# Kernel optimization log

Measured on AMD Instinct MI355X. Metric: run time of the kernel, lower is better.

Reference implementation:

```python
import jax, jax.numpy as jnp
import numpy as np

N, IN_RAW, H, E, UNROLLS = 1024, 10, 96, 16384, 2

def _p(key, shape):
    return jax.random.normal(key, shape, dtype=jnp.float32) * 0.05

def setup_inputs() -> dict:
    key = jax.random.key(0)
    ks = jax.random.split(key, 24)
    x = jax.random.normal(ks[0], (N, IN_RAW), dtype=jnp.float32)
    edge_index = jax.random.randint(ks[1], (2, E), 0, N, dtype=jnp.int64)
    adj = jax.random.randint(ks[2], (N, N), 0, 2, dtype=jnp.int32)
    return {
        'x': x, 'edge_index': edge_index, 'adj': adj,
        # init_layer
        'W_init': _p(ks[3], (H, IN_RAW - 1)), 'b_init': _p(ks[4], (H,)),
        # GatedGraphConv (num_layers=1): weight [H,H], GRUCell params
        'W_ggc': _p(ks[5], (H, H)),
        'W_ih': _p(ks[6], (3 * H, H)), 'W_hh': _p(ks[7], (3 * H, H)),
        'b_ih': _p(ks[8], (3 * H,)), 'b_hh': _p(ks[9], (3 * H,)),
        # edge_attention: Linear(2H->H), Linear(H->1)
        'Wa1': _p(ks[10], (H, 2 * H)), 'ba1': _p(ks[11], (H,)),
        'Wa2': _p(ks[12], (1, H)), 'ba2': _p(ks[13], (1,)),
        # out MLP
        'Wo1': _p(ks[14], (H, H)), 'bo1': _p(ks[15], (H,)),
        'Wo2': _p(ks[16], (H, H)), 'bo2': _p(ks[17], (H,)),
        # heads
        'Wp1': _p(ks[18], (1, H)), 'bp1': _p(ks[19], (1,)),
        'Wp2': _p(ks[20], (1, H)), 'bp2': _p(ks[21], (1,)),
    }

def _leaky(v):
    return jnp.where(v >= 0, v, 0.01 * v)  # LeakyReLU default slope

def _ggnn_forward(x, edge_index, adj,
                  W_init, b_init, W_ggc, W_ih, W_hh, b_ih, b_hh,
                  Wa1, ba1, Wa2, ba2, Wo1, bo1, Wo2, bo2,
                  Wp1, bp1, Wp2, bp2):
    src, tgt = edge_index[0], edge_index[1]
    x = x[:, :-1]                                   # data.x[:, :-1]
    x = _leaky(x @ W_init.T + b_init)               # [N,H]
    adj_mask = (adj == 1)
    for _ in range(UNROLLS):
        # GatedGraphConv, 1 layer, aggr='mean'
        m = x @ W_ggc                               # [N,H]
        s = jax.ops.segment_sum(m[src], tgt, num_segments=N)
        cnt = jax.ops.segment_sum(jnp.ones((E,), x.dtype), tgt, num_segments=N)
        agg = s / jnp.maximum(cnt, 1.0)[:, None]    # mean, 0 for isolated nodes
        # GRUCell(agg, x)
        gi = agg @ W_ih.T + b_ih
        gh = x @ W_hh.T + b_hh
        ir, iz, inn = jnp.split(gi, 3, axis=1)
        hr, hz, hn = jnp.split(gh, 3, axis=1)
        r = jax.nn.sigmoid(ir + hr)
        z = jax.nn.sigmoid(iz + hz)
        n = jnp.tanh(inn + r * hn)
        x = (1.0 - z) * n + z * x
        # edge attention: concat(x_i, x_j) -> Linear(2H->H) decomposed into
        # two [H,H] halves so the NxNx2H concat tensor is never materialized.
        hi = x @ Wa1[:, :H].T                       # acts on t1 (row i)
        hj = x @ Wa1[:, H:].T                       # acts on t2 (row j)
        h = jax.nn.sigmoid(hi[:, None, :] + hj[None, :, :] + ba1)  # [N,N,H]
        coeffs = jax.nn.sigmoid(h @ Wa2[0] + ba2[0])               # [N,N]
        coeffs = jnp.where(adj_mask, coeffs, 0.0)
        x = coeffs @ x
    x = _leaky(x @ Wo1.T + bo1)
    x = _leaky(x @ Wo2.T + bo2)
    out1 = jax.nn.sigmoid(x @ Wp1.T + bp1)
    out2 = jax.nn.sigmoid(x @ Wp2.T + bp2)
    return out1, out2

def reference(x, edge_index, adj,
              W_init, b_init, W_ggc, W_ih, W_hh, b_ih, b_hh,
              Wa1, ba1, Wa2, ba2, Wo1, bo1, Wo2, bo2,
              Wp1, bp1, Wp2, bp2):
    return _ggnn_forward(x, edge_index, adj,
                         W_init, b_init, W_ggc, W_ih, W_hh, b_ih, b_hh,
                         Wa1, ba1, Wa2, ba2, Wo1, bo1, Wo2, bo2,
                         Wp1, bp1, Wp2, bp2)
```

## Files before the change

kernel.cpp:

```cpp
#include <hip/hip_runtime.h>

#define Nn 1024
#define Hh 96
#define Ee 16384
#define IN_K 9
#define IN_STRIDE 10
#define NH (Nn * Hh)
#define XS 128
#define SLOTS 64

__device__ __forceinline__ float sigf(float v) {
    return __builtin_amdgcn_rcpf(1.0f + __expf(-v));
}
__device__ __forceinline__ float tanhfast(float v) {
    float e = __expf(2.0f * v);
    return (e - 1.0f) * __builtin_amdgcn_rcpf(e + 1.0f);
}
__device__ __forceinline__ float leakyf(float v) {
    return v >= 0.0f ? v : 0.01f * v;
}

__global__ __launch_bounds__(256) void setup1_kernel(
    const float* __restrict__ W_ih, const float* __restrict__ W_hh,
    const float* __restrict__ Wa1, const float* __restrict__ Wo1,
    const float* __restrict__ Wo2, const float* __restrict__ x_in,
    const float* __restrict__ W_init, const float* __restrict__ b_init,
    float* __restrict__ Wt_ih, float* __restrict__ Wt_hh,
    float* __restrict__ Wt_a1i, float* __restrict__ Wt_a1j,
    float* __restrict__ Wt_o1, float* __restrict__ Wt_o2,
    int* __restrict__ deg, float* __restrict__ xA)
{
    int gt = blockIdx.x * 256 + threadIdx.x;
    if (gt < Nn) deg[gt] = 0;
    if (gt < 92160) {
        int idx = gt;
        if (idx < 27648) {
            int k = idx / 288, c = idx % 288;
            Wt_ih[idx] = W_ih[c * 96 + k];
        } else if ((idx -= 27648) < 27648) {
            int k = idx / 288, c = idx % 288;
            Wt_hh[idx] = W_hh[c * 96 + k];
        } else if ((idx -= 27648) < 9216) {
            int k = idx / 96, h = idx % 96;
            Wt_a1i[idx] = Wa1[h * 192 + k];
        } else if ((idx -= 9216) < 9216) {
            int k = idx / 96, h = idx % 96;
            Wt_a1j[idx] = Wa1[h * 192 + 96 + k];
        } else if ((idx -= 9216) < 9216) {
            int k = idx / 96, j = idx % 96;
            Wt_o1[idx] = Wo1[j * 96 + k];
        } else {
            idx -= 9216;
            int k = idx / 96, j = idx % 96;
            Wt_o2[idx] = Wo2[j * 96 + k];
        }
    }
    if (gt < NH) {
        int n = gt / Hh, j = gt - n * Hh;
        const float* xr = x_in + n * IN_STRIDE;
        const float* wr = W_init + j * IN_K;
        float acc = b_init[j];
#pragma unroll
        for (int k = 0; k < IN_K; ++k) acc += xr[k] * wr[k];
        xA[n * XS + j] = leakyf(acc);
    }
}

__global__ __launch_bounds__(256) void setup2_kernel(
    const int* __restrict__ ei, const float* __restrict__ W_ggc,
    const float* __restrict__ Wt_ih,
    int* __restrict__ deg, int* __restrict__ bucket, float* __restrict__ Wf)
{
    int gt = blockIdx.x * 256 + threadIdx.x;
    if (gt < Ee) {
        int src = ei[gt];
        int tgt = ei[Ee + gt];
        int slot = atomicAdd(&deg[tgt], 1);
        if (slot < SLOTS) bucket[tgt * SLOTS + slot] = src;
    } else if (gt < Ee + 27648) {
        int idx = gt - Ee;
        int k = idx / 288, c = idx % 288;
        const float* g = W_ggc + k * 96;
        const float* w = Wt_ih + c;
        float acc = 0.0f;
        for (int j = 0; j < 96; ++j) acc += g[j] * w[j * 288];
        Wf[idx] = acc;
    }
}

__global__ __launch_bounds__(384) void gru_kernel(
    const float* __restrict__ xA, const int* __restrict__ deg,
    const int* __restrict__ bucket,
    const float* __restrict__ Wf, const float* __restrict__ Wt_hh,
    const float* __restrict__ b_ih, const float* __restrict__ b_hh,
    const float* __restrict__ Wt_a1i, const float* __restrict__ Wt_a1j,
    const float* __restrict__ ba1,
    float* __restrict__ xB, float* __restrict__ Ei, float* __restrict__ EjT)
{
    __shared__ float Pm[4][Hh];
    __shared__ float Xr[4][Hh];
    __shared__ float Xo[4][Hh];
    int tid = threadIdx.x;
    int r = tid / Hh, h = tid - r * Hh;
    int n = blockIdx.x * 4 + r;
    {
        int d = deg[n];
        int dc = d < SLOTS ? d : SLOTS;
        const int* bk = bucket + n * SLOTS;
        float acc = 0.0f;
        for (int s = 0; s < dc; ++s)
            acc += xA[bk[s] * XS + h];
        Pm[r][h] = acc * __builtin_amdgcn_rcpf(fmaxf((float)d, 1.0f));
        Xr[r][h] = xA[n * XS + h];
    }
    __syncthreads();
    {
        const float* Pr = Pm[r];
        const float* xr = Xr[r];
        const float* pf = Wf + h;
        const float* ph = Wt_hh + h;
        float gir = b_ih[h], giz = b_ih[Hh + h], gin = b_ih[2 * Hh + h];
        float ghr = b_hh[h], ghz = b_hh[Hh + h], ghn = b_hh[2 * Hh + h];
        for (int k = 0; k < Hh; ++k) {
            float a = Pr[k];
            float xv = xr[k];
            int o = k * 288;
            gir += a * pf[o];
            giz += a * pf[o + 96];
            gin += a * pf[o + 192];
            ghr += xv * ph[o];
            ghz += xv * ph[o + 96];
            ghn += xv * ph[o + 192];
        }
        float rr = sigf(gir + ghr);
        float z = sigf(giz + ghz);
        float nn2 = tanhfast(gin + rr * ghn);
        float xo = (1.0f - z) * nn2 + z * xr[h];
        xB[n * XS + h] = xo;
        Xo[r][h] = xo;
    }
    __syncthreads();
    {
        const float* row = Xo[r];
        const float* wi = Wt_a1i + h;
        const float* wj = Wt_a1j + h;
        float a = 0.0f, bb = 0.0f;
        for (int k = 0; k < Hh; ++k) {
            float xv = row[k];
            a += xv * wi[k * 96];
            bb += xv * wj[k * 96];
        }
        Ei[n * Hh + h] = __expf(-(a + ba1[h]));
        EjT[h * Nn + n] = __expf(-bb);
    }
}

#define SM_WA2 0
#define SM_EIS 96
#define SM_C   480
#define SM_RED 4576
__global__ __launch_bounds__(512) void attn_kernel(
    const float* __restrict__ Ei, const float* __restrict__ EjT,
    const float* __restrict__ Wa2, const float* __restrict__ ba2,
    const int* __restrict__ adj, const float* __restrict__ xB,
    float* __restrict__ xA)
{
    __shared__ float sm[4576 + 1536];
    int tid = threadIdx.x;
    int i0 = blockIdx.x * 4;
    if (tid < Hh) sm[SM_WA2 + tid] = Wa2[tid];
    if (tid < 4 * Hh) {
        int r = tid / Hh, h = tid - r * Hh;
        sm[SM_EIS + tid] = Ei[(i0 + r) * Hh + h];
    }
    __syncthreads();
    {
        int j2 = tid * 2;
        float a0 = 0.f, a1 = 0.f, a2 = 0.f, a3 = 0.f;
        float b0 = 0.f, b1 = 0.f, b2_ = 0.f, b3 = 0.f;
        const float* eis = sm + SM_EIS;
#pragma unroll 2
        for (int k = 0; k < Hh; ++k) {
            float2 e = *(const float2*)(EjT + k * Nn + j2);
            float wk = sm[SM_WA2 + k];
            float e0 = eis[k];
            float e1 = eis[96 + k];
            float e2 = eis[192 + k];
            float e3 = eis[288 + k];
            a0 += __builtin_amdgcn_rcpf(fmaf(e0, e.x, 1.0f)) * wk;
            b0 += __builtin_amdgcn_rcpf(fmaf(e0, e.y, 1.0f)) * wk;
            a1 += __builtin_amdgcn_rcpf(fmaf(e1, e.x, 1.0f)) * wk;
            b1 += __builtin_amdgcn_rcpf(fmaf(e1, e.y, 1.0f)) * wk;
            a2 += __builtin_amdgcn_rcpf(fmaf(e2, e.x, 1.0f)) * wk;
            b2_ += __builtin_amdgcn_rcpf(fmaf(e2, e.y, 1.0f)) * wk;
            a3 += __builtin_amdgcn_rcpf(fmaf(e3, e.x, 1.0f)) * wk;
            b3 += __builtin_amdgcn_rcpf(fmaf(e3, e.y, 1.0f)) * wk;
        }
        float bb = ba2[0];
        int2 m0 = *(const int2*)(adj + (i0 + 0) * Nn + j2);
        int2 m1 = *(const int2*)(adj + (i0 + 1) * Nn + j2);
        int2 m2 = *(const int2*)(adj + (i0 + 2) * Nn + j2);
        int2 m3 = *(const int2*)(adj + (i0 + 3) * Nn + j2);
        sm[SM_C + 0 * Nn + j2]     = (m0.x == 1) ? sigf(a0 + bb) : 0.0f;
        sm[SM_C + 0 * Nn + j2 + 1] = (m0.y == 1) ? sigf(b0 + bb) : 0.0f;
        sm[SM_C + 1 * Nn + j2]     = (m1.x == 1) ? sigf(a1 + bb) : 0.0f;
        sm[SM_C + 1 * Nn + j2 + 1] = (m1.y == 1) ? sigf(b1 + bb) : 0.0f;
        sm[SM_C + 2 * Nn + j2]     = (m2.x == 1) ? sigf(a2 + bb) : 0.0f;
        sm[SM_C + 2 * Nn + j2 + 1] = (m2.y == 1) ? sigf(b2_ + bb) : 0.0f;
        sm[SM_C + 3 * Nn + j2]     = (m3.x == 1) ? sigf(a3 + bb) : 0.0f;
        sm[SM_C + 3 * Nn + j2 + 1] = (m3.y == 1) ? sigf(b3 + bb) : 0.0f;
    }
    __syncthreads();
    {
        int q = tid >> 7;
        int h = tid & 127;
        float acc0 = 0.f, acc1 = 0.f, acc2 = 0.f, acc3 = 0.f;
        if (h < Hh) {
            const float* xc = xB + h;
            int jb = q * 256;
            const float* c0 = sm + SM_C + 0 * Nn + jb;
            const float* c1 = sm + SM_C + 1 * Nn + jb;
            const float* c2 = sm + SM_C + 2 * Nn + jb;
            const float* c3 = sm + SM_C + 3 * Nn + jb;
#pragma unroll 4
            for (int j = 0; j < 256; ++j) {
                float xv = xc[(jb + j) * XS];
                acc0 += c0[j] * xv;
                acc1 += c1[j] * xv;
                acc2 += c2[j] * xv;
                acc3 += c3[j] * xv;
            }
            sm[SM_RED + (q * 4 + 0) * Hh + h] = acc0;
            sm[SM_RED + (q * 4 + 1) * Hh + h] = acc1;
            sm[SM_RED + (q * 4 + 2) * Hh + h] = acc2;
            sm[SM_RED + (q * 4 + 3) * Hh + h] = acc3;
        }
        __syncthreads();
        if (q == 0 && h < Hh) {
#pragma unroll
            for (int r = 0; r < 4; ++r) {
                float v = sm[SM_RED + r * Hh + h]
                        + sm[SM_RED + (4 + r) * Hh + h]
                        + sm[SM_RED + (8 + r) * Hh + h]
                        + sm[SM_RED + (12 + r) * Hh + h];
                xA[(i0 + r) * XS + h] = v;
            }
        }
    }
}

__global__ __launch_bounds__(384) void head_kernel(
    const float* __restrict__ xA,
    const float* __restrict__ Wt_o1, const float* __restrict__ bo1,
    const float* __restrict__ Wt_o2, const float* __restrict__ bo2,
    const float* __restrict__ Wp1, const float* __restrict__ bp1,
    const float* __restrict__ Wp2, const float* __restrict__ bp2,
    float* __restrict__ out)
{
    __shared__ float xr[4][Hh];
    __shared__ float t1[4][Hh];
    __shared__ float t2[4][Hh];
    int tid = threadIdx.x;
    int r = tid / Hh, h = tid - r * Hh;
    int n = blockIdx.x * 4 + r;
    xr[r][h] = xA[n * XS + h];
    __syncthreads();
    {
        const float* w = Wt_o1 + h;
        float acc = bo1[h];
        for (int k = 0; k < Hh; ++k) acc += xr[r][k] * w[k * 96];
        t1[r][h] = leakyf(acc);
    }
    __syncthreads();
    {
        const float* w = Wt_o2 + h;
        float acc = bo2[h];
        for (int k = 0; k < Hh; ++k) acc += t1[r][k] * w[k * 96];
        t2[r][h] = leakyf(acc);
    }
    __syncthreads();
    if (h == 0) {
        float s1 = 0.f;
        for (int k = 0; k < Hh; ++k) s1 += t2[r][k] * Wp1[k];
        out[n] = sigf(s1 + bp1[0]);
    } else if (h == 1) {
        float s2 = 0.f;
        for (int k = 0; k < Hh; ++k) s2 += t2[r][k] * Wp2[k];
        out[Nn + n] = sigf(s2 + bp2[0]);
    }
}

extern "C" void kernel_launch(void* const* d_in, const int* in_sizes, int n_in,
                              void* d_out, int out_size, void* d_ws, size_t ws_size,
                              hipStream_t stream)
{
    const float* x_in   = (const float*)d_in[0];
    const int*   ei     = (const int*)d_in[1];
    const int*   adj    = (const int*)d_in[2];
    const float* W_init = (const float*)d_in[3];
    const float* b_init = (const float*)d_in[4];
    const float* W_ggc  = (const float*)d_in[5];
    const float* W_ih   = (const float*)d_in[6];
    const float* W_hh   = (const float*)d_in[7];
    const float* b_ih   = (const float*)d_in[8];
    const float* b_hh   = (const float*)d_in[9];
    const float* Wa1    = (const float*)d_in[10];
    const float* ba1    = (const float*)d_in[11];
    const float* Wa2    = (const float*)d_in[12];
    const float* ba2    = (const float*)d_in[13];
    const float* Wo1    = (const float*)d_in[14];
    const float* bo1    = (const float*)d_in[15];
    const float* Wo2    = (const float*)d_in[16];
    const float* bo2    = (const float*)d_in[17];
    const float* Wp1    = (const float*)d_in[18];
    const float* bp1    = (const float*)d_in[19];
    const float* Wp2    = (const float*)d_in[20];
    const float* bp2    = (const float*)d_in[21];
    float* out = (float*)d_out;

    float* ws     = (float*)d_ws;
    float* xA     = ws;
    float* xB     = xA + Nn * XS;
    float* Ei     = xB + Nn * XS;
    float* EjT    = Ei + NH;
    float* Wt_ih  = EjT + NH;
    float* Wt_hh  = Wt_ih + 27648;
    float* Wf     = Wt_hh + 27648;
    float* Wt_a1i = Wf + 27648;
    float* Wt_a1j = Wt_a1i + 9216;
    float* Wt_o1  = Wt_a1j + 9216;
    float* Wt_o2  = Wt_o1 + 9216;
    int*   deg    = (int*)(Wt_o2 + 9216);
    int*   bucket = deg + Nn;

    setup1_kernel<<<(NH + 255) / 256, 256, 0, stream>>>(
        W_ih, W_hh, Wa1, Wo1, Wo2, x_in, W_init, b_init,
        Wt_ih, Wt_hh, Wt_a1i, Wt_a1j, Wt_o1, Wt_o2, deg, xA);
    setup2_kernel<<<(Ee + 27648 + 255) / 256, 256, 0, stream>>>(
        ei, W_ggc, Wt_ih, deg, bucket, Wf);

    for (int u = 0; u < 2; ++u) {
        gru_kernel<<<Nn / 4, 384, 0, stream>>>(
            xA, deg, bucket, Wf, Wt_hh, b_ih, b_hh,
            Wt_a1i, Wt_a1j, ba1, xB, Ei, EjT);
        attn_kernel<<<Nn / 4, 512, 0, stream>>>(
            Ei, EjT, Wa2, ba2, adj, xB, xA);
    }

    head_kernel<<<Nn / 4, 384, 0, stream>>>(
        xA, Wt_o1, bo1, Wt_o2, bo2, Wp1, bp1, Wp2, bp2, out);
}
```

Baseline: 227.8 us.

## Halve rows per block, split GRU reductions, fuse head into attention kernel

Each GRU and attention block now handles 2 nodes instead of 4, so 512 blocks launch instead of 256. The GRU kernel splits its K-reductions and neighbour gathers across two thread halves, combined through shared memory. The head MLP is fused into the final attention launch through a template flag, and Wf is computed directly from W_ih, so the transposed Wt_ih pass and one dependency are dropped. This is meant to raise occupancy and parallelism and cut launch count. In exchange it adds extra syncs and shared-memory reductions, and each EjT load is now reused across 2 rows instead of 4.

```diff
diff --git a/kernel.cpp b/kernel.cpp
--- a/kernel.cpp
+++ b/kernel.cpp
@@ -20,24 +20,22 @@
     return v >= 0.0f ? v : 0.01f * v;
 }
 
-__global__ __launch_bounds__(256) void setup1_kernel(
-    const float* __restrict__ W_ih, const float* __restrict__ W_hh,
-    const float* __restrict__ Wa1, const float* __restrict__ Wo1,
-    const float* __restrict__ Wo2, const float* __restrict__ x_in,
-    const float* __restrict__ W_init, const float* __restrict__ b_init,
-    float* __restrict__ Wt_ih, float* __restrict__ Wt_hh,
-    float* __restrict__ Wt_a1i, float* __restrict__ Wt_a1j,
-    float* __restrict__ Wt_o1, float* __restrict__ Wt_o2,
+__global__ __launch_bounds__(256) void setup_kernel(
+    const float* __restrict__ W_hh, const float* __restrict__ Wa1,
+    const float* __restrict__ Wo1, const float* __restrict__ Wo2,
+    const float* __restrict__ W_ggc, const float* __restrict__ W_ih,
+    const float* __restrict__ x_in, const float* __restrict__ W_init,
+    const float* __restrict__ b_init,
+    float* __restrict__ Wt_hh, float* __restrict__ Wt_a1i,
+    float* __restrict__ Wt_a1j, float* __restrict__ Wt_o1,
+    float* __restrict__ Wt_o2, float* __restrict__ Wf,
     int* __restrict__ deg, float* __restrict__ xA)
 {
     int gt = blockIdx.x * 256 + threadIdx.x;
     if (gt < Nn) deg[gt] = 0;
-    if (gt < 92160) {
+    if (gt < 64512) {
         int idx = gt;
         if (idx < 27648) {
-            int k = idx / 288, c = idx % 288;
-            Wt_ih[idx] = W_ih[c * 96 + k];
-        } else if ((idx -= 27648) < 27648) {
             int k = idx / 288, c = idx % 288;
             Wt_hh[idx] = W_hh[c * 96 + k];
         } else if ((idx -= 27648) < 9216) {
@@ -55,6 +53,14 @@
             Wt_o2[idx] = Wo2[j * 96 + k];
         }
     }
+    if (gt < 27648) {
+        int k = gt / 288, c = gt % 288;
+        const float* g = W_ggc + k * 96;
+        const float* w = W_ih + c * 96;
+        float acc = 0.0f;
+        for (int j = 0; j < 96; ++j) acc += g[j] * w[j];
+        Wf[gt] = acc;
+    }
     if (gt < NH) {
         int n = gt / Hh, j = gt - n * Hh;
         const float* xr = x_in + n * IN_STRIDE;
@@ -66,26 +72,15 @@
     }
 }
 
-__global__ __launch_bounds__(256) void setup2_kernel(
-    const int* __restrict__ ei, const float* __restrict__ W_ggc,
-    const float* __restrict__ Wt_ih,
-    int* __restrict__ deg, int* __restrict__ bucket, float* __restrict__ Wf)
-{
-    int gt = blockIdx.x * 256 + threadIdx.x;
-    if (gt < Ee) {
-        int src = ei[gt];
-        int tgt = ei[Ee + gt];
-        int slot = atomicAdd(&deg[tgt], 1);
-        if (slot < SLOTS) bucket[tgt * SLOTS + slot] = src;
-    } else if (gt < Ee + 27648) {
-        int idx = gt - Ee;
-        int k = idx / 288, c = idx % 288;
-        const float* g = W_ggc + k * 96;
-        const float* w = Wt_ih + c;
-        float acc = 0.0f;
-        for (int j = 0; j < 96; ++j) acc += g[j] * w[j * 288];
-        Wf[idx] = acc;
-    }
+__global__ __launch_bounds__(256) void edges_kernel(
+    const int* __restrict__ ei, int* __restrict__ deg, int* __restrict__ bucket)
+{
+    int e = blockIdx.x * 256 + threadIdx.x;
+    if (e >= Ee) return;
+    int src = ei[e];
+    int tgt = ei[Ee + e];
+    int slot = atomicAdd(&deg[tgt], 1);
+    if (slot < SLOTS) bucket[tgt * SLOTS + slot] = src;
 }
 
 __global__ __launch_bounds__(384) void gru_kernel(
@@ -97,21 +92,31 @@
     const float* __restrict__ ba1,
     float* __restrict__ xB, float* __restrict__ Ei, float* __restrict__ EjT)
 {
-    __shared__ float Pm[4][Hh];
-    __shared__ float Xr[4][Hh];
-    __shared__ float Xo[4][Hh];
+    __shared__ float Pp[2][2][Hh];
+    __shared__ float Pm[2][Hh];
+    __shared__ float Xr[2][Hh];
+    __shared__ float Xo[2][Hh];
+    __shared__ float red6[2][2][Hh][6];
+    __shared__ float redp[2][2][Hh][2];
     int tid = threadIdx.x;
-    int r = tid / Hh, h = tid - r * Hh;
-    int n = blockIdx.x * 4 + r;
+    int half = tid / 192;
+    int loc = tid - half * 192;
+    int r = loc / Hh, h = loc - r * Hh;
+    int n = blockIdx.x * 2 + r;
     {
         int d = deg[n];
         int dc = d < SLOTS ? d : SLOTS;
         const int* bk = bucket + n * SLOTS;
         float acc = 0.0f;
-        for (int s = 0; s < dc; ++s)
+        for (int s = half; s < dc; s += 2)
             acc += xA[bk[s] * XS + h];
-        Pm[r][h] = acc * __builtin_amdgcn_rcpf(fmaxf((float)d, 1.0f));
-        Xr[r][h] = xA[n * XS + h];
+        Pp[half][r][h] = acc;
+        if (half == 0) Xr[r][h] = xA[n * XS + h];
+    }
+    __syncthreads();
+    if (half == 0) {
+        float inv = __builtin_amdgcn_rcpf(fmaxf((float)deg[n], 1.0f));
+        Pm[r][h] = (Pp[0][r][h] + Pp[1][r][h]) * inv;
     }
     __syncthreads();
     {
@@ -119,9 +124,11 @@
         const float* xr = Xr[r];
         const float* pf = Wf + h;
         const float* ph = Wt_hh + h;
-        float gir = b_ih[h], giz = b_ih[Hh + h], gin = b_ih[2 * Hh + h];
-        float ghr = b_hh[h], ghz = b_hh[Hh + h], ghn = b_hh[2 * Hh + h];
-        for (int k = 0; k < Hh; ++k) {
+        float gir = 0.f, giz = 0.f, gin = 0.f;
+        float ghr = 0.f, ghz = 0.f, ghn = 0.f;
+        int k0 = half * 48;
+#pragma unroll 4
+        for (int k = k0; k < k0 + 48; ++k) {
             float a = Pr[k];
             float xv = xr[k];
             int o = k * 288;
@@ -132,10 +139,25 @@
             ghz += xv * ph[o + 96];
             ghn += xv * ph[o + 192];
         }
+        red6[half][r][h][0] = gir;
+        red6[half][r][h][1] = giz;
+        red6[half][r][h][2] = gin;
+        red6[half][r][h][3] = ghr;
+        red6[half][r][h][4] = ghz;
+        red6[half][r][h][5] = ghn;
+    }
+    __syncthreads();
+    if (half == 0) {
+        float gir = b_ih[h] + red6[0][r][h][0] + red6[1][r][h][0];
+        float giz = b_ih[Hh + h] + red6[0][r][h][1] + red6[1][r][h][1];
+        float gin = b_ih[2 * Hh + h] + red6[0][r][h][2] + red6[1][r][h][2];
+        float ghr = b_hh[h] + red6[0][r][h][3] + red6[1][r][h][3];
+        float ghz = b_hh[Hh + h] + red6[0][r][h][4] + red6[1][r][h][4];
+        float ghn = b_hh[2 * Hh + h] + red6[0][r][h][5] + red6[1][r][h][5];
         float rr = sigf(gir + ghr);
         float z = sigf(giz + ghz);
         float nn2 = tanhfast(gin + rr * ghn);
-        float xo = (1.0f - z) * nn2 + z * xr[h];
+        float xo = (1.0f - z) * nn2 + z * Xr[r][h];
         xB[n * XS + h] = xo;
         Xo[r][h] = xo;
     }
@@ -145,148 +167,131 @@
         const float* wi = Wt_a1i + h;
         const float* wj = Wt_a1j + h;
         float a = 0.0f, bb = 0.0f;
-        for (int k = 0; k < Hh; ++k) {
+        int k0 = half * 48;
+#pragma unroll 4
+        for (int k = k0; k < k0 + 48; ++k) {
             float xv = row[k];
             a += xv * wi[k * 96];
             bb += xv * wj[k * 96];
         }
+        redp[half][r][h][0] = a;
+        redp[half][r][h][1] = bb;
+    }
+    __syncthreads();
+    if (half == 0) {
+        float a = redp[0][r][h][0] + redp[1][r][h][0];
+        float bb = redp[0][r][h][1] + redp[1][r][h][1];
         Ei[n * Hh + h] = __expf(-(a + ba1[h]));
         EjT[h * Nn + n] = __expf(-bb);
     }
 }
 
-#define SM_WA2 0
-#define SM_EIS 96
-#define SM_C   480
-#define SM_RED 4576
+template <bool HEAD>
 __global__ __launch_bounds__(512) void attn_kernel(
     const float* __restrict__ Ei, const float* __restrict__ EjT,
     const float* __restrict__ Wa2, const float* __restrict__ ba2,
     const int* __restrict__ adj, const float* __restrict__ xB,
-    float* __restrict__ xA)
-{
-    __shared__ float sm[4576 + 1536];
+    float* __restrict__ xA,
+    const float* __restrict__ Wt_o1, const float* __restrict__ bo1,
+    const float* __restrict__ Wt_o2, const float* __restrict__ bo2,
+    const float* __restrict__ Wp1, const float* __restrict__ bp1,
+    const float* __restrict__ Wp2, const float* __restrict__ bp2,
+    float* __restrict__ out)
+{
+    __shared__ __align__(16) float wa2[Hh];
+    __shared__ __align__(16) float eis[2][Hh];
+    __shared__ __align__(16) float C[2][Nn];
+    __shared__ float red[4][2][Hh];
+    __shared__ float xout[2][Hh];
+    __shared__ float t1[2][Hh];
+    __shared__ float t2[2][Hh];
     int tid = threadIdx.x;
-    int i0 = blockIdx.x * 4;
-    if (tid < Hh) sm[SM_WA2 + tid] = Wa2[tid];
-    if (tid < 4 * Hh) {
+    int i0 = blockIdx.x * 2;
+    if (tid < Hh) wa2[tid] = Wa2[tid];
+    if (tid < 2 * Hh) {
         int r = tid / Hh, h = tid - r * Hh;
-        sm[SM_EIS + tid] = Ei[(i0 + r) * Hh + h];
-    }
-    __syncthreads();
-    {
-        int j2 = tid * 2;
-        float a0 = 0.f, a1 = 0.f, a2 = 0.f, a3 = 0.f;
-        float b0 = 0.f, b1 = 0.f, b2_ = 0.f, b3 = 0.f;
-        const float* eis = sm + SM_EIS;
-#pragma unroll 2
+        eis[r][h] = Ei[(i0 + r) * Hh + h];
+    }
+    __syncthreads();
+    {
+        int row = tid >> 8;
+        int jj = (tid & 255) * 4;
+        int4 mk = *(const int4*)(adj + (i0 + row) * Nn + jj);
+        float s0 = 0.f, s1 = 0.f, s2 = 0.f, s3 = 0.f;
+        const float* er = eis[row];
+#pragma unroll 4
         for (int k = 0; k < Hh; ++k) {
-            float2 e = *(const float2*)(EjT + k * Nn + j2);
-            float wk = sm[SM_WA2 + k];
-            float e0 = eis[k];
-            float e1 = eis[96 + k];
-            float e2 = eis[192 + k];
-            float e3 = eis[288 + k];
-            a0 += __builtin_amdgcn_rcpf(fmaf(e0, e.x, 1.0f)) * wk;
-            b0 += __builtin_amdgcn_rcpf(fmaf(e0, e.y, 1.0f)) * wk;
-            a1 += __builtin_amdgcn_rcpf(fmaf(e1, e.x, 1.0f)) * wk;
-            b1 += __builtin_amdgcn_rcpf(fmaf(e1, e.y, 1.0f)) * wk;
-            a2 += __builtin_amdgcn_rcpf(fmaf(e2, e.x, 1.0f)) * wk;
-            b2_ += __builtin_amdgcn_rcpf(fmaf(e2, e.y, 1.0f)) * wk;
-            a3 += __builtin_amdgcn_rcpf(fmaf(e3, e.x, 1.0f)) * wk;
-            b3 += __builtin_amdgcn_rcpf(fmaf(e3, e.y, 1.0f)) * wk;
-        }
-        float bb = ba2[0];
-        int2 m0 = *(const int2*)(adj + (i0 + 0) * Nn + j2);
-        int2 m1 = *(const int2*)(adj + (i0 + 1) * Nn + j2);
-        int2 m2 = *(const int2*)(adj + (i0 + 2) * Nn + j2);
-        int2 m3 = *(const int2*)(adj + (i0 + 3) * Nn + j2);
-        sm[SM_C + 0 * Nn + j2]     = (m0.x == 1) ? sigf(a0 + bb) : 0.0f;
-        sm[SM_C + 0 * Nn + j2 + 1] = (m0.y == 1) ? sigf(b0 + bb) : 0.0f;
-        sm[SM_C + 1 * Nn + j2]     = (m1.x == 1) ? sigf(a1 + bb) : 0.0f;
-        sm[SM_C + 1 * Nn + j2 + 1] = (m1.y == 1) ? sigf(b1 + bb) : 0.0f;
-        sm[SM_C + 2 * Nn + j2]     = (m2.x == 1) ? sigf(a2 + bb) : 0.0f;
-        sm[SM_C + 2 * Nn + j2 + 1] = (m2.y == 1) ? sigf(b2_ + bb) : 0.0f;
-        sm[SM_C + 3 * Nn + j2]     = (m3.x == 1) ? sigf(a3 + bb) : 0.0f;
-        sm[SM_C + 3 * Nn + j2 + 1] = (m3.y == 1) ? sigf(b3 + bb) : 0.0f;
+            float4 e4 = *(const float4*)(EjT + k * Nn + jj);
+            float eik = er[k];
+            float wk = wa2[k];
+            s0 += __builtin_amdgcn_rcpf(fmaf(eik, e4.x, 1.0f)) * wk;
+            s1 += __builtin_amdgcn_rcpf(fmaf(eik, e4.y, 1.0f)) * wk;
+            s2 += __builtin_amdgcn_rcpf(fmaf(eik, e4.z, 1.0f)) * wk;
+            s3 += __builtin_amdgcn_rcpf(fmaf(eik, e4.w, 1.0f)) * wk;
+        }
+        float b2 = ba2[0];
+        float4 c;
+        c.x = (mk.x == 1) ? sigf(s0 + b2) : 0.0f;
+        c.y = (mk.y == 1) ? sigf(s1 + b2) : 0.0f;
+        c.z = (mk.z == 1) ? sigf(s2 + b2) : 0.0f;
+        c.w = (mk.w == 1) ? sigf(s3 + b2) : 0.0f;
+        *(float4*)(&C[row][jj]) = c;
     }
     __syncthreads();
     {
         int q = tid >> 7;
         int h = tid & 127;
-        float acc0 = 0.f, acc1 = 0.f, acc2 = 0.f, acc3 = 0.f;
         if (h < Hh) {
             const float* xc = xB + h;
             int jb = q * 256;
-            const float* c0 = sm + SM_C + 0 * Nn + jb;
-            const float* c1 = sm + SM_C + 1 * Nn + jb;
-            const float* c2 = sm + SM_C + 2 * Nn + jb;
-            const float* c3 = sm + SM_C + 3 * Nn + jb;
+            const float* c0 = &C[0][jb];
+            const float* c1 = &C[1][jb];
+            float acc0 = 0.f, acc1 = 0.f;
 #pragma unroll 4
             for (int j = 0; j < 256; ++j) {
                 float xv = xc[(jb + j) * XS];
                 acc0 += c0[j] * xv;
                 acc1 += c1[j] * xv;
-                acc2 += c2[j] * xv;
-                acc3 += c3[j] * xv;
             }
-            sm[SM_RED + (q * 4 + 0) * Hh + h] = acc0;
-            sm[SM_RED + (q * 4 + 1) * Hh + h] = acc1;
-            sm[SM_RED + (q * 4 + 2) * Hh + h] = acc2;
-            sm[SM_RED + (q * 4 + 3) * Hh + h] = acc3;
+            red[q][0][h] = acc0;
+            red[q][1][h] = acc1;
         }
         __syncthreads();
         if (q == 0 && h < Hh) {
 #pragma unroll
-            for (int r = 0; r < 4; ++r) {
-                float v = sm[SM_RED + r * Hh + h]
-                        + sm[SM_RED + (4 + r) * Hh + h]
-                        + sm[SM_RED + (8 + r) * Hh + h]
-                        + sm[SM_RED + (12 + r) * Hh + h];
-                xA[(i0 + r) * XS + h] = v;
+            for (int r = 0; r < 2; ++r) {
+                float v = red[0][r][h] + red[1][r][h] + red[2][r][h] + red[3][r][h];
+                if (HEAD) xout[r][h] = v;
+                else      xA[(i0 + r) * XS + h] = v;
             }
         }
     }
-}
-
-__global__ __launch_bounds__(384) void head_kernel(
-    const float* __restrict__ xA,
-    const float* __restrict__ Wt_o1, const float* __restrict__ bo1,
-    const float* __restrict__ Wt_o2, const float* __restrict__ bo2,
-    const float* __restrict__ Wp1, const float* __restrict__ bp1,
-    const float* __restrict__ Wp2, const float* __restrict__ bp2,
-    float* __restrict__ out)
-{
-    __shared__ float xr[4][Hh];
-    __shared__ float t1[4][Hh];
-    __shared__ float t2[4][Hh];
-    int tid = threadIdx.x;
-    int r = tid / Hh, h = tid - r * Hh;
-    int n = blockIdx.x * 4 + r;
-    xr[r][h] = xA[n * XS + h];
-    __syncthreads();
-    {
-        const float* w = Wt_o1 + h;
-        float acc = bo1[h];
-        for (int k = 0; k < Hh; ++k) acc += xr[r][k] * w[k * 96];
-        t1[r][h] = leakyf(acc);
-    }
-    __syncthreads();
-    {
-        const float* w = Wt_o2 + h;
-        float acc = bo2[h];
-        for (int k = 0; k < Hh; ++k) acc += t1[r][k] * w[k * 96];
-        t2[r][h] = leakyf(acc);
-    }
-    __syncthreads();
-    if (h == 0) {
-        float s1 = 0.f;
-        for (int k = 0; k < Hh; ++k) s1 += t2[r][k] * Wp1[k];
-        out[n] = sigf(s1 + bp1[0]);
-    } else if (h == 1) {
-        float s2 = 0.f;
-        for (int k = 0; k < Hh; ++k) s2 += t2[r][k] * Wp2[k];
-        out[Nn + n] = sigf(s2 + bp2[0]);
+    if (HEAD) {
+        __syncthreads();
+        if (tid < 2 * Hh) {
+            int r = tid / Hh, h = tid - r * Hh;
+            const float* w = Wt_o1 + h;
+            float acc = bo1[h];
+            for (int k = 0; k < Hh; ++k) acc += xout[r][k] * w[k * 96];
+            t1[r][h] = leakyf(acc);
+        }
+        __syncthreads();
+        if (tid < 2 * Hh) {
+            int r = tid / Hh, h = tid - r * Hh;
+            const float* w = Wt_o2 + h;
+            float acc = bo2[h];
+            for (int k = 0; k < Hh; ++k) acc += t1[r][k] * w[k * 96];
+            t2[r][h] = leakyf(acc);
+        }
+        __syncthreads();
+        if (tid < 4) {
+            int r = tid >> 1, which = tid & 1;
+            const float* wp = which ? Wp2 : Wp1;
+            float acc = 0.f;
+            for (int k = 0; k < Hh; ++k) acc += t2[r][k] * wp[k];
+            float b = which ? bp2[0] : bp1[0];
+            out[which * Nn + i0 + r] = sigf(acc + b);
+        }
     }
 }
 
@@ -323,8 +328,7 @@
     float* xB     = xA + Nn * XS;
     float* Ei     = xB + Nn * XS;
     float* EjT    = Ei + NH;
-    float* Wt_ih  = EjT + NH;
-    float* Wt_hh  = Wt_ih + 27648;
+    float* Wt_hh  = EjT + NH;
     float* Wf     = Wt_hh + 27648;
     float* Wt_a1i = Wf + 27648;
     float* Wt_a1j = Wt_a1i + 9216;
@@ -333,20 +337,22 @@
     int*   deg    = (int*)(Wt_o2 + 9216);
     int*   bucket = deg + Nn;
 
-    setup1_kernel<<<(NH + 255) / 256, 256, 0, stream>>>(
-        W_ih, W_hh, Wa1, Wo1, Wo2, x_in, W_init, b_init,
-        Wt_ih, Wt_hh, Wt_a1i, Wt_a1j, Wt_o1, Wt_o2, deg, xA);
-    setup2_kernel<<<(Ee + 27648 + 255) / 256, 256, 0, stream>>>(
-        ei, W_ggc, Wt_ih, deg, bucket, Wf);
-
-    for (int u = 0; u < 2; ++u) {
-        gru_kernel<<<Nn / 4, 384, 0, stream>>>(
-            xA, deg, bucket, Wf, Wt_hh, b_ih, b_hh,
-            Wt_a1i, Wt_a1j, ba1, xB, Ei, EjT);
-        attn_kernel<<<Nn / 4, 512, 0, stream>>>(
-            Ei, EjT, Wa2, ba2, adj, xB, xA);
-    }
-
-    head_kernel<<<Nn / 4, 384, 0, stream>>>(
-        xA, Wt_o1, bo1, Wt_o2, bo2, Wp1, bp1, Wp2, bp2, out);
-}
+    setup_kernel<<<(NH + 255) / 256, 256, 0, stream>>>(
+        W_hh, Wa1, Wo1, Wo2, W_ggc, W_ih, x_in, W_init, b_init,
+        Wt_hh, Wt_a1i, Wt_a1j, Wt_o1, Wt_o2, Wf, deg, xA);
+    edges_kernel<<<(Ee + 255) / 256, 256, 0, stream>>>(ei, deg, bucket);
+
+    gru_kernel<<<Nn / 2, 384, 0, stream>>>(
+        xA, deg, bucket, Wf, Wt_hh, b_ih, b_hh, Wt_a1i, Wt_a1j, ba1,
+        xB, Ei, EjT);
+    attn_kernel<false><<<Nn / 2, 512, 0, stream>>>(
+        Ei, EjT, Wa2, ba2, adj, xB, xA,
+        nullptr, nullptr, nullptr, nullptr, nullptr, nullptr, nullptr, nullptr,
+        nullptr);
+    gru_kernel<<<Nn / 2, 384, 0, stream>>>(
+        xA, deg, bucket, Wf, Wt_hh, b_ih, b_hh, Wt_a1i, Wt_a1j, ba1,
+        xB, Ei, EjT);
+    attn_kernel<true><<<Nn / 2, 512, 0, stream>>>(
+        Ei, EjT, Wa2, ba2, adj, xB, xA,
+        Wt_o1, bo1, Wt_o2, bo2, Wp1, bp1, Wp2, bp2, out);
+}
```

Result: faster. 211.3 us (-7.2%).
